# Kernel optimization log

Measured on AMD Instinct MI355X. Metric: run time of the kernel, lower is better.

## Reference

```python
import jax, jax.numpy as jnp
import numpy as np

B, N, L = 32, 1024, 128
K, D_E, H = 3, 16, 4


def setup_inputs() -> dict:
    key = jax.random.key(0)
    ks = jax.random.split(key, 7)
    return {
        "x": jax.random.normal(ks[0], (B, N, L), jnp.float32),
        # mild scaling on embeddings/projections keeps softmax logits in a sane range
        "psi_emb": jax.random.normal(ks[1], (N, D_E), jnp.float32) * 0.3,
        "psi": jnp.float32(1.0),
        "W_q": jax.random.normal(ks[2], (D_E, H, D_E), jnp.float32) * 0.2,
        "W_k": jax.random.normal(ks[3], (D_E, H, D_E), jnp.float32) * 0.2,
        "attn_alpha": jnp.float32(0.5),
        "F_w": jax.random.normal(ks[4], (H, D_E, K + 1, L), jnp.float32) * 0.1,
        "f_b": jax.random.normal(ks[5], (H, D_E), jnp.float32),
        "head_mix": jnp.ones((H,), jnp.float32),
    }


def reference(x, psi_emb, psi, W_q, W_k, attn_alpha, F_w, f_b, head_mix):
    # x: (B, N, L)
    n = x.shape[1]
    # --- gaussian adjacency: softmax over columns of exp(-psi * ||psi_i - psi_j||^2)
    diff = psi_emb[:, None, :] - psi_emb[None, :, :]          # (N, N, d_e)
    dist2 = jnp.sum(diff * diff, axis=-1)                     # (N, N)
    A_base = jax.nn.softmax(jnp.exp(-psi * dist2), axis=1)    # (N, N)
    # --- per-head attention adjacency
    Q = jnp.einsum('nd,dhm->nhm', psi_emb, W_q)               # (N, H, d_e)
    Kt = jnp.einsum('nd,dhm->nhm', psi_emb, W_k)              # (N, H, d_e)
    scale = 1.0 / jnp.sqrt(jnp.asarray(Q.shape[-1], x.dtype))
    A_attn = jax.nn.softmax(
        jnp.einsum('nhd,mhd->hnm', Q, Kt) * scale, axis=-1)   # (H, N, N)
    # --- sigmoid blend (all heads at once)
    alpha = jax.nn.sigmoid(attn_alpha)
    A_eff = alpha * A_base[None] + (1.0 - alpha) * A_attn     # (H, N, N)
    # --- Chebyshev recursion: T0 = I, T1 = A, Tk = 2 A T_{k-1} - T_{k-2}
    I = jnp.broadcast_to(jnp.eye(n, dtype=x.dtype), A_eff.shape)
    supports = [I, A_eff]
    for _ in range(2, K + 1):
        supports.append(2.0 * jnp.einsum('hnm,hml->hnl', A_eff, supports[-1]) - supports[-2])
    S = jnp.stack(supports, axis=1)                           # (H, K+1, N, N)
    # --- per-node filters
    W_filter = jnp.einsum('nd,hdkl->hnkl', psi_emb, F_w)      # (H, N, K+1, L)
    b_filter = jnp.einsum('nd,hd->hn', psi_emb, f_b)          # (H, N)
    # --- graph conv + node-specific contraction
    x_g = jnp.einsum('hknm,bml->bhknl', S, x)                 # (B, H, K+1, N, L)
    out_h = jnp.einsum('bhknl,hnkl->bhn', x_g, W_filter) + b_filter[None]
    # --- head mixing
    mix_w = jax.nn.softmax(head_mix, axis=0)                  # (H,)
    return jnp.einsum('bhn,h->bn', out_h, mix_w)              # (B, N)
```

## Files before the change

### kernel.cpp

```cpp
#include <hip/hip_runtime.h>
#include <cstdint>

#define NN 1024
#define BB 32
#define LL 128
#define DE 16
#define HH 4
#define K1 4
#define BD 512
#define NS 524288

using bf16x8 = __attribute__((ext_vector_type(8))) short;
using f32x4  = __attribute__((ext_vector_type(4))) float;

__device__ inline unsigned short f2bf(float f) {
    unsigned u = __builtin_bit_cast(unsigned, f);
    u += 0x7FFFu + ((u >> 16) & 1u);
    return (unsigned short)(u >> 16);
}
__device__ inline float bf2f(unsigned short u) {
    return __builtin_bit_cast(float, (unsigned)u << 16);
}

struct LogitsSmem {
    float ejs[64][17];
    float eis[64][17];
    float kjs[64][64];
    float qis[4][64][17];
    float part[4][5][64];
    float wq[1024];
    float wk[1024];
};
struct XtSmem { float xs[64][128]; };

__global__ __launch_bounds__(256) void phase1(
    const float* __restrict__ psi_emb, const float* __restrict__ psi_p,
    const float* __restrict__ W_q, const float* __restrict__ W_k,
    const float* __restrict__ x, const float* __restrict__ F_w,
    short* __restrict__ bnt, short* __restrict__ ant, float* __restrict__ partials,
    short* __restrict__ xt, short* __restrict__ wtt, float* __restrict__ out)
{
    __shared__ __align__(16) char smem_raw[sizeof(LogitsSmem)];
    const int bid = blockIdx.x;
    const int tid = threadIdx.x;

    if (bid < 256) {
        LogitsSmem& S = *(LogitsSmem*)smem_raw;
        const int jb = bid & 15, ib = bid >> 4;
        const int i0 = ib * 64, j0 = jb * 64;
        {
            const int row = tid >> 2, dq = (tid & 3) * 4;
            const float4 vj = *(const float4*)(psi_emb + (j0 + row) * DE + dq);
            S.ejs[row][dq] = vj.x; S.ejs[row][dq + 1] = vj.y;
            S.ejs[row][dq + 2] = vj.z; S.ejs[row][dq + 3] = vj.w;
            const float4 vi = *(const float4*)(psi_emb + (i0 + row) * DE + dq);
            S.eis[row][dq] = vi.x; S.eis[row][dq + 1] = vi.y;
            S.eis[row][dq + 2] = vi.z; S.eis[row][dq + 3] = vi.w;
            *(float4*)&S.wq[tid * 4] = *(const float4*)(W_q + tid * 4);
            *(float4*)&S.wk[tid * 4] = *(const float4*)(W_k + tid * 4);
        }
        __syncthreads();
#pragma unroll
        for (int rep = 0; rep < 16; rep++) {
            const int idx = rep * 256 + tid;
            const int row = idx >> 6, hm = idx & 63;
            float qv = 0.f, kv = 0.f;
#pragma unroll
            for (int d = 0; d < DE; d++) {
                qv += S.eis[row][d] * S.wq[d * 64 + hm];
                kv += S.ejs[row][d] * S.wk[d * 64 + hm];
            }
            S.qis[hm >> 4][row][hm & 15] = qv;
            S.kjs[row][hm] = kv;
        }
        __syncthreads();

        const int i = tid & 63, jg = tid >> 6;
        const float psi = psi_p[0];
        float er[DE];
#pragma unroll
        for (int d = 0; d < DE; d++) er[d] = S.eis[i][d];

        float sb = 0.f, sa[HH] = {0.f, 0.f, 0.f, 0.f};
#pragma unroll
        for (int g = 0; g < 2; g++) {
            unsigned short bw[8];
#pragma unroll
            for (int r = 0; r < 8; r++) {
                const int j = jg * 16 + g * 8 + r;
                float d2 = 0.f;
#pragma unroll
                for (int d = 0; d < DE; d++) { const float t = er[d] - S.ejs[j][d]; d2 += t * t; }
                const float bn = __expf(__expf(-psi * d2));
                sb += bn;
                bw[r] = f2bf(bn);
            }
            uint4 pk;
            pk.x = bw[0] | ((unsigned)bw[1] << 16);
            pk.y = bw[2] | ((unsigned)bw[3] << 16);
            pk.z = bw[4] | ((unsigned)bw[5] << 16);
            pk.w = bw[6] | ((unsigned)bw[7] << 16);
            const size_t toff = (size_t)((j0 + jg * 16 + g * 8) >> 3) * 8192 + (size_t)(i0 + i) * 8;
            *(uint4*)(bnt + toff) = pk;
        }
#pragma unroll
        for (int h = 0; h < HH; h++) {
            float qr[DE];
#pragma unroll
            for (int m = 0; m < DE; m++) qr[m] = S.qis[h][i][m];
#pragma unroll
            for (int g = 0; g < 2; g++) {
                unsigned short aw[8];
#pragma unroll
                for (int r = 0; r < 8; r++) {
                    const int j = jg * 16 + g * 8 + r;
                    float dot = 0.f;
#pragma unroll
                    for (int m = 0; m < DE; m++) dot += qr[m] * S.kjs[j][h * DE + m];
                    const float an = __expf(dot * 0.25f);
                    sa[h] += an;
                    aw[r] = f2bf(an);
                }
                uint4 pk;
                pk.x = aw[0] | ((unsigned)aw[1] << 16);
                pk.y = aw[2] | ((unsigned)aw[3] << 16);
                pk.z = aw[4] | ((unsigned)aw[5] << 16);
                pk.w = aw[6] | ((unsigned)aw[7] << 16);
                const size_t toff = (size_t)((j0 + jg * 16 + g * 8) >> 3) * 8192 + (size_t)(i0 + i) * 8;
                *(uint4*)(ant + (size_t)h * 1048576 + toff) = pk;
            }
        }
        S.part[jg][0][i] = sb;
#pragma unroll
        for (int h = 0; h < HH; h++) S.part[jg][1 + h][i] = sa[h];
        __syncthreads();
        if (tid < 64) {
#pragma unroll
            for (int s = 0; s < 5; s++) {
                const float v = S.part[0][s][tid] + S.part[1][s][tid] +
                                S.part[2][s][tid] + S.part[3][s][tid];
                partials[(size_t)jb * 5120 + (size_t)s * 1024 + i0 + tid] = v;
            }
        }
    } else if (bid < 768) {
        XtSmem& X = *(XtSmem*)smem_raw;
        const int idx = bid - 256;
        const int m0 = (idx & 15) * 64;
        const int b  = idx >> 4;
        for (int i = tid; i < 2048; i += 256) {
            const int row = i >> 5, lq = i & 31;
            *(float4*)&X.xs[row][lq * 4] =
                *(const float4*)(x + ((size_t)(b * NN + m0 + row)) * LL + lq * 4);
        }
        __syncthreads();
        for (int j = tid; j < 1024; j += 256) {
            const int m = j & 63, lc = j >> 6;
            const float* s = &X.xs[m][lc * 8];
            uint4 pk;
            pk.x = f2bf(s[0]) | ((unsigned)f2bf(s[1]) << 16);
            pk.y = f2bf(s[2]) | ((unsigned)f2bf(s[3]) << 16);
            pk.z = f2bf(s[4]) | ((unsigned)f2bf(s[5]) << 16);
            pk.w = f2bf(s[6]) | ((unsigned)f2bf(s[7]) << 16);
            *(uint4*)(xt + (size_t)b * 131072 + (size_t)lc * 8192 + (size_t)(m0 + m) * 8) = pk;
        }
    } else if (bid < 784) {
        const int j = (bid - 768) * 256 + tid;
        const int lc = j >> 8, c = j & 255;
        const int h = c >> 6, k = (c >> 4) & 3, d = c & 15;
        const float* s = F_w + (size_t)((h * DE + d) * K1 + k) * LL + lc * 8;
        uint4 pk;
        pk.x = f2bf(s[0]) | ((unsigned)f2bf(s[1]) << 16);
        pk.y = f2bf(s[2]) | ((unsigned)f2bf(s[3]) << 16);
        pk.z = f2bf(s[4]) | ((unsigned)f2bf(s[5]) << 16);
        pk.w = f2bf(s[6]) | ((unsigned)f2bf(s[7]) << 16);
        *(uint4*)(wtt + (size_t)lc * 2048 + (size_t)c * 8) = pk;
    } else {
        const int idx = (bid - 784) * 256 + tid;
        const float4 z = {0.f, 0.f, 0.f, 0.f};
        *(float4*)(out + (size_t)idx * 8) = z;
        *(float4*)(out + (size_t)idx * 8 + 4) = z;
    }
}

__global__ __launch_bounds__(256) void phase2(
    const short* __restrict__ xt, const short* __restrict__ wtt,
    short* __restrict__ Gt,
    const short* __restrict__ bnt, const short* __restrict__ ant,
    const float* __restrict__ partials, const float* __restrict__ alpha_p,
    short* __restrict__ At)
{
    const int bid = blockIdx.x;
    const int tid = threadIdx.x;
    __shared__ float sums_l[5][64];

    if (bid < 1024) {
        const int cb = bid & 3;
        const int m0 = ((bid >> 2) & 15) * 64;
        const int bp = bid >> 6;
        const int wave = tid >> 6, lane = tid & 63;
        const int b  = bp * 2 + (wave >> 1);
        const int wc = wave & 1;
        const int q = lane >> 4, m16 = lane & 15;
        const short* xb = xt + (size_t)b * 131072;

        f32x4 acc[4][2];
#pragma unroll
        for (int mi = 0; mi < 4; mi++)
#pragma unroll
            for (int ni = 0; ni < 2; ni++) acc[mi][ni] = (f32x4){0.f, 0.f, 0.f, 0.f};

#pragma unroll
        for (int ks = 0; ks < 4; ks++) {
            const int kc = ks * 4 + q;
            bf16x8 a[4], bb[2];
#pragma unroll
            for (int mi = 0; mi < 4; mi++)
                a[mi] = *(const bf16x8*)(xb + (size_t)kc * 8192 + (size_t)(m0 + mi * 16 + m16) * 8);
#pragma unroll
            for (int ni = 0; ni < 2; ni++)
                bb[ni] = *(const bf16x8*)(wtt + (size_t)kc * 2048 +
                                          (size_t)(cb * 64 + wc * 32 + ni * 16 + m16) * 8);
#pragma unroll
            for (int mi = 0; mi < 4; mi++)
#pragma unroll
                for (int ni = 0; ni < 2; ni++)
                    acc[mi][ni] = __builtin_amdgcn_mfma_f32_16x16x32_bf16(a[mi], bb[ni], acc[mi][ni], 0, 0, 0);
        }

#pragma unroll
        for (int ni = 0; ni < 2; ni++) {
            const int cc = cb * 64 + wc * 32 + ni * 16 + m16;
            const int kk = (cc >> 4) & 3, hh = cc >> 6;
            const int col512 = b * 16 + (cc & 15);
            short* gdst = Gt + (size_t)(kk * 4 + hh) * 524288;
#pragma unroll
            for (int mi = 0; mi < 4; mi++) {
                const int row0 = m0 + mi * 16 + q * 4;
                ushort4 pk;
                pk.x = f2bf(acc[mi][ni][0]); pk.y = f2bf(acc[mi][ni][1]);
                pk.z = f2bf(acc[mi][ni][2]); pk.w = f2bf(acc[mi][ni][3]);
                *(ushort4*)(gdst + ((size_t)(row0 >> 3) * 512 + col512) * 8 + (row0 & 7)) = pk;
            }
        }
    } else {
        const int idx = bid - 1024;
        const int jb = idx & 15, ib = idx >> 4;
        const int i0 = ib * 64, j0 = jb * 64;
        const int lane = tid & 63, w = tid >> 6;
        {
            float acc = 0.f;
#pragma unroll
            for (int jb2 = 0; jb2 < 16; jb2++)
                acc += partials[(size_t)jb2 * 5120 + (size_t)w * 1024 + i0 + lane];
            sums_l[w][lane] = acc;
            if (w == 0) {
                float a4 = 0.f;
#pragma unroll
                for (int jb2 = 0; jb2 < 16; jb2++)
                    a4 += partials[(size_t)jb2 * 5120 + 4 * 1024 + i0 + lane];
                sums_l[4][lane] = a4;
            }
        }
        __syncthreads();
        const int i = lane, jg = w;
        const float alpha = 1.f / (1.f + __expf(-alpha_p[0]));
        const float ibs = alpha / sums_l[0][i];
        float ias[HH];
#pragma unroll
        for (int h = 0; h < HH; h++) ias[h] = (1.f - alpha) / sums_l[1 + h][i];

#pragma unroll
        for (int g = 0; g < 2; g++) {
            const size_t toff = (size_t)((j0 + jg * 16 + g * 8) >> 3) * 8192 + (size_t)(i0 + i) * 8;
            const uint4 bp = *(const uint4*)(bnt + toff);
            float bnv[8];
            bnv[0] = bf2f(bp.x & 0xFFFF); bnv[1] = bf2f(bp.x >> 16);
            bnv[2] = bf2f(bp.y & 0xFFFF); bnv[3] = bf2f(bp.y >> 16);
            bnv[4] = bf2f(bp.z & 0xFFFF); bnv[5] = bf2f(bp.z >> 16);
            bnv[6] = bf2f(bp.w & 0xFFFF); bnv[7] = bf2f(bp.w >> 16);
#pragma unroll
            for (int h = 0; h < HH; h++) {
                const uint4 ap = *(const uint4*)(ant + (size_t)h * 1048576 + toff);
                float av[8];
                av[0] = bf2f(ap.x & 0xFFFF); av[1] = bf2f(ap.x >> 16);
                av[2] = bf2f(ap.y & 0xFFFF); av[3] = bf2f(ap.y >> 16);
                av[4] = bf2f(ap.z & 0xFFFF); av[5] = bf2f(ap.z >> 16);
                av[6] = bf2f(ap.w & 0xFFFF); av[7] = bf2f(ap.w >> 16);
                unsigned short ow[8];
#pragma unroll
                for (int r = 0; r < 8; r++) ow[r] = f2bf(ibs * bnv[r] + ias[h] * av[r]);
                uint4 pk;
                pk.x = ow[0] | ((unsigned)ow[1] << 16);
                pk.y = ow[2] | ((unsigned)ow[3] << 16);
                pk.z = ow[4] | ((unsigned)ow[5] << 16);
                pk.w = ow[6] | ((unsigned)ow[7] << 16);
                *(uint4*)(At + (size_t)h * 1048576 + toff) = pk;
            }
        }
    }
}

__global__ __launch_bounds__(256) void gemm_mf(
    const short* __restrict__ At, const short* __restrict__ Bt,
    const short* __restrict__ Pt, const short* __restrict__ Qt,
    short* __restrict__ Ot, float scale, float pc, float qc)
{
    const int bid = blockIdx.x;
    const int h = (bid & 7) >> 1;
    const int tile = ((bid >> 3) << 1) | (bid & 1);
    const int c0 = (tile & 7) * 64;
    const int r0 = (tile >> 3) * 64;

    const short* Ah = At + (size_t)h * 1048576;
    const short* Bh = Bt + (size_t)h * 524288;
    const short* Ph = Pt + (size_t)h * 524288;
    const short* Qh = Qt + (size_t)h * 524288;
    short* Oh = Ot + (size_t)h * 524288;

    const int tid = threadIdx.x;
    const int wave = tid >> 6, lane = tid & 63;
    const int q = lane >> 4, m16 = lane & 15;
    const int wr = wave >> 1, wc = wave & 1;

    const short* Ap = Ah + (size_t)q * 8192 + (size_t)(r0 + wr * 32 + m16) * 8;
    const short* Bp = Bh + (size_t)q * 4096 + (size_t)(c0 + wc * 32 + m16) * 8;

    f32x4 acc[2][2];
#pragma unroll
    for (int mi = 0; mi < 2; mi++)
#pragma unroll
        for (int ni = 0; ni < 2; ni++) acc[mi][ni] = (f32x4){0.f, 0.f, 0.f, 0.f};

#pragma unroll 8
    for (int it = 0; it < 32; it++) {
        const bf16x8 af0 = *(const bf16x8*)(Ap + (size_t)it * 32768);
        const bf16x8 af1 = *(const bf16x8*)(Ap + (size_t)it * 32768 + 128);
        const bf16x8 bf0 = *(const bf16x8*)(Bp + (size_t)it * 16384);
        const bf16x8 bf1 = *(const bf16x8*)(Bp + (size_t)it * 16384 + 128);
        acc[0][0] = __builtin_amdgcn_mfma_f32_16x16x32_bf16(af0, bf0, acc[0][0], 0, 0, 0);
        acc[0][1] = __builtin_amdgcn_mfma_f32_16x16x32_bf16(af0, bf1, acc[0][1], 0, 0, 0);
        acc[1][0] = __builtin_amdgcn_mfma_f32_16x16x32_bf16(af1, bf0, acc[1][0], 0, 0, 0);
        acc[1][1] = __builtin_amdgcn_mfma_f32_16x16x32_bf16(af1, bf1, acc[1][1], 0, 0, 0);
    }

#pragma unroll
    for (int mi = 0; mi < 2; mi++) {
        const int row0 = r0 + wr * 32 + mi * 16 + q * 4;
#pragma unroll
        for (int ni = 0; ni < 2; ni++) {
            const int cc = c0 + wc * 32 + ni * 16 + m16;
            const size_t off = ((size_t)(row0 >> 3) * 512 + cc) * 8 + (row0 & 7);
            const ushort4 pv = *(const ushort4*)(Ph + off);
            float v[4];
            v[0] = scale * acc[mi][ni][0] + pc * bf2f(pv.x);
            v[1] = scale * acc[mi][ni][1] + pc * bf2f(pv.y);
            v[2] = scale * acc[mi][ni][2] + pc * bf2f(pv.z);
            v[3] = scale * acc[mi][ni][3] + pc * bf2f(pv.w);
            if (qc != 0.f) {
                const ushort4 qv = *(const ushort4*)(Qh + off);
                v[0] += qc * bf2f(qv.x); v[1] += qc * bf2f(qv.y);
                v[2] += qc * bf2f(qv.z); v[3] += qc * bf2f(qv.w);
            }
            ushort4 pk;
            pk.x = f2bf(v[0]); pk.y = f2bf(v[1]); pk.z = f2bf(v[2]); pk.w = f2bf(v[3]);
            *(ushort4*)(Oh + off) = pk;
        }
    }
}

__global__ __launch_bounds__(256) void gemm3_out(
    const short* __restrict__ At, const short* __restrict__ Bt,
    const short* __restrict__ Pt, const short* __restrict__ Qt,
    const float* __restrict__ psi_emb, const float* __restrict__ f_b,
    const float* __restrict__ head_mix, float* __restrict__ out)
{
    const int bid = blockIdx.x;
    const int h = (bid & 7) >> 1;
    const int tile = ((bid >> 3) << 1) | (bid & 1);
    const int c0 = (tile & 7) * 64;
    const int r0 = (tile >> 3) * 64;

    const short* Ah = At + (size_t)h * 1048576;
    const short* Bh = Bt + (size_t)h * 524288;
    const short* Ph = Pt + (size_t)h * 524288;
    const short* Qh = Qt + (size_t)h * 524288;

    const int tid = threadIdx.x;
    const int wave = tid >> 6, lane = tid & 63;
    const int q = lane >> 4, m16 = lane & 15;
    const int wr = wave >> 1, wc = wave & 1;

    __shared__ float es[64][17];
    {
        const int row = tid >> 2, dq = (tid & 3) * 4;
        const float4 ev = *(const float4*)(psi_emb + (size_t)(r0 + row) * DE + dq);
        es[row][dq] = ev.x; es[row][dq + 1] = ev.y;
        es[row][dq + 2] = ev.z; es[row][dq + 3] = ev.w;
    }
    __syncthreads();

    const short* Ap = Ah + (size_t)q * 8192 + (size_t)(r0 + wr * 32 + m16) * 8;
    const short* Bp = Bh + (size_t)q * 4096 + (size_t)(c0 + wc * 32 + m16) * 8;

    f32x4 acc[2][2];
#pragma unroll
    for (int mi = 0; mi < 2; mi++)
#pragma unroll
        for (int ni = 0; ni < 2; ni++) acc[mi][ni] = (f32x4){0.f, 0.f, 0.f, 0.f};

#pragma unroll 8
    for (int it = 0; it < 32; it++) {
        const bf16x8 af0 = *(const bf16x8*)(Ap + (size_t)it * 32768);
        const bf16x8 af1 = *(const bf16x8*)(Ap + (size_t)it * 32768 + 128);
        const bf16x8 bf0 = *(const bf16x8*)(Bp + (size_t)it * 16384);
        const bf16x8 bf1 = *(const bf16x8*)(Bp + (size_t)it * 16384 + 128);
        acc[0][0] = __builtin_amdgcn_mfma_f32_16x16x32_bf16(af0, bf0, acc[0][0], 0, 0, 0);
        acc[0][1] = __builtin_amdgcn_mfma_f32_16x16x32_bf16(af0, bf1, acc[0][1], 0, 0, 0);
        acc[1][0] = __builtin_amdgcn_mfma_f32_16x16x32_bf16(af1, bf0, acc[1][0], 0, 0, 0);
        acc[1][1] = __builtin_amdgcn_mfma_f32_16x16x32_bf16(af1, bf1, acc[1][1], 0, 0, 0);
    }

    const float hm0 = head_mix[0], hm1 = head_mix[1], hm2 = head_mix[2], hm3 = head_mix[3];
    const float mx = fmaxf(fmaxf(hm0, hm1), fmaxf(hm2, hm3));
    const float w0 = expf(hm0 - mx), w1 = expf(hm1 - mx), w2 = expf(hm2 - mx), w3 = expf(hm3 - mx);
    const float isum = 1.f / (w0 + w1 + w2 + w3);
    const float mwh = (h == 0 ? w0 : h == 1 ? w1 : h == 2 ? w2 : w3) * isum;
    const float fb = f_b[h * DE + m16];

#pragma unroll
    for (int mi = 0; mi < 2; mi++) {
        const int rloc0 = wr * 32 + mi * 16 + q * 4;
        const int row0 = r0 + rloc0;
#pragma unroll
        for (int ni = 0; ni < 2; ni++) {
            const int cc = c0 + wc * 32 + ni * 16 + m16;
            const int b = cc >> 4;
            const size_t off = ((size_t)(row0 >> 3) * 512 + cc) * 8 + (row0 & 7);
            const ushort4 pv = *(const ushort4*)(Ph + off);
            const ushort4 qv = *(const ushort4*)(Qh + off);
            float v[4];
            v[0] = acc[mi][ni][0] + bf2f(pv.x) - bf2f(qv.x);
            v[1] = acc[mi][ni][1] + bf2f(pv.y) - bf2f(qv.y);
            v[2] = acc[mi][ni][2] + bf2f(pv.z) - bf2f(qv.z);
            v[3] = acc[mi][ni][3] + bf2f(pv.w) - bf2f(qv.w);
#pragma unroll
            for (int r = 0; r < 4; r++) {
                float w = es[rloc0 + r][m16] * (v[r] + fb);
                w += __shfl_xor(w, 1, 64);
                w += __shfl_xor(w, 2, 64);
                w += __shfl_xor(w, 4, 64);
                w += __shfl_xor(w, 8, 64);
                if (m16 == 0)
                    atomicAdd(out + (size_t)b * NN + (row0 + r), mwh * w);
            }
        }
    }
}

extern "C" void kernel_launch(void* const* d_in, const int* in_sizes, int n_in,
                              void* d_out, int out_size, void* d_ws, size_t ws_size,
                              hipStream_t stream)
{
    const float* x          = (const float*)d_in[0];
    const float* psi_emb    = (const float*)d_in[1];
    const float* psi        = (const float*)d_in[2];
    const float* W_q        = (const float*)d_in[3];
    const float* W_k        = (const float*)d_in[4];
    const float* attn_alpha = (const float*)d_in[5];
    const float* F_w        = (const float*)d_in[6];
    const float* f_b        = (const float*)d_in[7];
    const float* head_mix   = (const float*)d_in[8];
    float* out = (float*)d_out;

    short* At  = (short*)d_ws;
    short* xt  = At + 4194304;
    short* wtt = xt + 4194304;
    short* Gt  = wtt + 32768;
    short* b2t = Gt + 8388608;
    short* b1t = b2t + 2097152;
    short* bnt = b1t + 2097152;
    short* ant = bnt + 1048576;
    float* partials = (float*)(ant + 4194304);

    const size_t need_bytes =
        (size_t)(4194304 + 4194304 + 32768 + 8388608 + 2097152 + 2097152 + 1048576 + 4194304) * 2 +
        (size_t)81920 * 4;
    if (ws_size < need_bytes) return;

    phase1<<<800, 256, 0, stream>>>(psi_emb, psi, W_q, W_k, x, F_w,
                                    bnt, ant, partials, xt, wtt, out);
    phase2<<<1280, 256, 0, stream>>>(xt, wtt, Gt, bnt, ant, partials,
                                     attn_alpha, At);

    gemm_mf<<<512, 256, 0, stream>>>(At, Gt + 12 * (size_t)524288, Gt + 8 * (size_t)524288,
                                     Gt , b2t, 2.f, 1.f, 0.f);
    gemm_mf<<<512, 256, 0, stream>>>(At, b2t, Gt + 4 * (size_t)524288,
                                     Gt + 12 * (size_t)524288, b1t, 2.f, 1.f, -1.f);
    gemm3_out<<<512, 256, 0, stream>>>(At, b1t, Gt, b2t, psi_emb, f_b, head_mix, out);
}
```

Measured before the change: 148.6 us.

## Fuse three Clenshaw GEMM launches into one cooperative kernel with grid syncs

Replaces the two gemm_mf launches and the final gemm3_out launch with one cooperative kernel. It runs the three A·B products back to back and separates them with grid-wide barriers. The goal is to remove kernel launch gaps and tail effects between the dependent steps. The cost is grid.sync overhead, and the cooperative launch needs all 512 blocks resident at once, or it fails.

```diff
diff --git a/kernel.cpp b/kernel.cpp
--- a/kernel.cpp
+++ b/kernel.cpp
@@ -1,5 +1,8 @@
 #include <hip/hip_runtime.h>
+#include <hip/hip_cooperative_groups.h>
 #include <cstdint>
+
+namespace cg = cooperative_groups;
 
 #define NN 1024
 #define BB 32
@@ -8,7 +11,7 @@
 #define HH 4
 #define K1 4
 #define BD 512
-#define NS 524288
+#define SLAB 524288
 
 using bf16x8 = __attribute__((ext_vector_type(8))) short;
 using f32x4  = __attribute__((ext_vector_type(4))) float;
@@ -232,7 +235,7 @@
             const int cc = cb * 64 + wc * 32 + ni * 16 + m16;
             const int kk = (cc >> 4) & 3, hh = cc >> 6;
             const int col512 = b * 16 + (cc & 15);
-            short* gdst = Gt + (size_t)(kk * 4 + hh) * 524288;
+            short* gdst = Gt + (size_t)(kk * 4 + hh) * SLAB;
 #pragma unroll
             for (int mi = 0; mi < 4; mi++) {
                 const int row0 = m0 + mi * 16 + q * 4;
@@ -300,37 +303,11 @@
     }
 }
 
-__global__ __launch_bounds__(256) void gemm_mf(
-    const short* __restrict__ At, const short* __restrict__ Bt,
-    const short* __restrict__ Pt, const short* __restrict__ Qt,
-    short* __restrict__ Ot, float scale, float pc, float qc)
-{
-    const int bid = blockIdx.x;
-    const int h = (bid & 7) >> 1;
-    const int tile = ((bid >> 3) << 1) | (bid & 1);
-    const int c0 = (tile & 7) * 64;
-    const int r0 = (tile >> 3) * 64;
-
-    const short* Ah = At + (size_t)h * 1048576;
-    const short* Bh = Bt + (size_t)h * 524288;
-    const short* Ph = Pt + (size_t)h * 524288;
-    const short* Qh = Qt + (size_t)h * 524288;
-    short* Oh = Ot + (size_t)h * 524288;
-
-    const int tid = threadIdx.x;
-    const int wave = tid >> 6, lane = tid & 63;
-    const int q = lane >> 4, m16 = lane & 15;
-    const int wr = wave >> 1, wc = wave & 1;
-
-    const short* Ap = Ah + (size_t)q * 8192 + (size_t)(r0 + wr * 32 + m16) * 8;
-    const short* Bp = Bh + (size_t)q * 4096 + (size_t)(c0 + wc * 32 + m16) * 8;
-
-    f32x4 acc[2][2];
+__device__ inline void k_loop(const short* Ap, const short* Bp, f32x4 acc[2][2]) {
 #pragma unroll
     for (int mi = 0; mi < 2; mi++)
 #pragma unroll
         for (int ni = 0; ni < 2; ni++) acc[mi][ni] = (f32x4){0.f, 0.f, 0.f, 0.f};
-
 #pragma unroll 8
     for (int it = 0; it < 32; it++) {
         const bf16x8 af0 = *(const bf16x8*)(Ap + (size_t)it * 32768);
@@ -342,53 +319,31 @@
         acc[1][0] = __builtin_amdgcn_mfma_f32_16x16x32_bf16(af1, bf0, acc[1][0], 0, 0, 0);
         acc[1][1] = __builtin_amdgcn_mfma_f32_16x16x32_bf16(af1, bf1, acc[1][1], 0, 0, 0);
     }
-
-#pragma unroll
-    for (int mi = 0; mi < 2; mi++) {
-        const int row0 = r0 + wr * 32 + mi * 16 + q * 4;
-#pragma unroll
-        for (int ni = 0; ni < 2; ni++) {
-            const int cc = c0 + wc * 32 + ni * 16 + m16;
-            const size_t off = ((size_t)(row0 >> 3) * 512 + cc) * 8 + (row0 & 7);
-            const ushort4 pv = *(const ushort4*)(Ph + off);
-            float v[4];
-            v[0] = scale * acc[mi][ni][0] + pc * bf2f(pv.x);
-            v[1] = scale * acc[mi][ni][1] + pc * bf2f(pv.y);
-            v[2] = scale * acc[mi][ni][2] + pc * bf2f(pv.z);
-            v[3] = scale * acc[mi][ni][3] + pc * bf2f(pv.w);
-            if (qc != 0.f) {
-                const ushort4 qv = *(const ushort4*)(Qh + off);
-                v[0] += qc * bf2f(qv.x); v[1] += qc * bf2f(qv.y);
-                v[2] += qc * bf2f(qv.z); v[3] += qc * bf2f(qv.w);
-            }
-            ushort4 pk;
-            pk.x = f2bf(v[0]); pk.y = f2bf(v[1]); pk.z = f2bf(v[2]); pk.w = f2bf(v[3]);
-            *(ushort4*)(Oh + off) = pk;
-        }
-    }
-}
-
-__global__ __launch_bounds__(256) void gemm3_out(
-    const short* __restrict__ At, const short* __restrict__ Bt,
-    const short* __restrict__ Pt, const short* __restrict__ Qt,
+}
+
+__global__ __launch_bounds__(256) void clenshaw_chain(
+    const short* __restrict__ At, const short* __restrict__ Gt,
+    short* b2t, short* b1t,
     const float* __restrict__ psi_emb, const float* __restrict__ f_b,
     const float* __restrict__ head_mix, float* __restrict__ out)
 {
+    cg::grid_group grid = cg::this_grid();
+
     const int bid = blockIdx.x;
     const int h = (bid & 7) >> 1;
     const int tile = ((bid >> 3) << 1) | (bid & 1);
     const int c0 = (tile & 7) * 64;
     const int r0 = (tile >> 3) * 64;
 
-    const short* Ah = At + (size_t)h * 1048576;
-    const short* Bh = Bt + (size_t)h * 524288;
-    const short* Ph = Pt + (size_t)h * 524288;
-    const short* Qh = Qt + (size_t)h * 524288;
-
     const int tid = threadIdx.x;
     const int wave = tid >> 6, lane = tid & 63;
     const int q = lane >> 4, m16 = lane & 15;
     const int wr = wave >> 1, wc = wave & 1;
+
+    const size_t hs = (size_t)h * SLAB;
+    const short* Ap = At + (size_t)h * 1048576 +
+                      (size_t)q * 8192 + (size_t)(r0 + wr * 32 + m16) * 8;
+    const size_t bofs = (size_t)q * 4096 + (size_t)(c0 + wc * 32 + m16) * 8;
 
     __shared__ float es[64][17];
     {
@@ -399,26 +354,50 @@
     }
     __syncthreads();
 
-    const short* Ap = Ah + (size_t)q * 8192 + (size_t)(r0 + wr * 32 + m16) * 8;
-    const short* Bp = Bh + (size_t)q * 4096 + (size_t)(c0 + wc * 32 + m16) * 8;
-
     f32x4 acc[2][2];
-#pragma unroll
-    for (int mi = 0; mi < 2; mi++)
-#pragma unroll
-        for (int ni = 0; ni < 2; ni++) acc[mi][ni] = (f32x4){0.f, 0.f, 0.f, 0.f};
-
-#pragma unroll 8
-    for (int it = 0; it < 32; it++) {
-        const bf16x8 af0 = *(const bf16x8*)(Ap + (size_t)it * 32768);
-        const bf16x8 af1 = *(const bf16x8*)(Ap + (size_t)it * 32768 + 128);
-        const bf16x8 bf0 = *(const bf16x8*)(Bp + (size_t)it * 16384);
-        const bf16x8 bf1 = *(const bf16x8*)(Bp + (size_t)it * 16384 + 128);
-        acc[0][0] = __builtin_amdgcn_mfma_f32_16x16x32_bf16(af0, bf0, acc[0][0], 0, 0, 0);
-        acc[0][1] = __builtin_amdgcn_mfma_f32_16x16x32_bf16(af0, bf1, acc[0][1], 0, 0, 0);
-        acc[1][0] = __builtin_amdgcn_mfma_f32_16x16x32_bf16(af1, bf0, acc[1][0], 0, 0, 0);
-        acc[1][1] = __builtin_amdgcn_mfma_f32_16x16x32_bf16(af1, bf1, acc[1][1], 0, 0, 0);
-    }
+
+    k_loop(Ap, Gt + (12 + h) * (size_t)SLAB + bofs, acc);
+#pragma unroll
+    for (int mi = 0; mi < 2; mi++) {
+        const int row0 = r0 + wr * 32 + mi * 16 + q * 4;
+#pragma unroll
+        for (int ni = 0; ni < 2; ni++) {
+            const int cc = c0 + wc * 32 + ni * 16 + m16;
+            const size_t off = ((size_t)(row0 >> 3) * 512 + cc) * 8 + (row0 & 7);
+            const ushort4 pv = *(const ushort4*)(Gt + (8 + h) * (size_t)SLAB + off);
+            ushort4 pk;
+            pk.x = f2bf(2.f * acc[mi][ni][0] + bf2f(pv.x));
+            pk.y = f2bf(2.f * acc[mi][ni][1] + bf2f(pv.y));
+            pk.z = f2bf(2.f * acc[mi][ni][2] + bf2f(pv.z));
+            pk.w = f2bf(2.f * acc[mi][ni][3] + bf2f(pv.w));
+            *(ushort4*)(b2t + hs + off) = pk;
+        }
+    }
+    __threadfence();
+    grid.sync();
+
+    k_loop(Ap, b2t + hs + bofs, acc);
+#pragma unroll
+    for (int mi = 0; mi < 2; mi++) {
+        const int row0 = r0 + wr * 32 + mi * 16 + q * 4;
+#pragma unroll
+        for (int ni = 0; ni < 2; ni++) {
+            const int cc = c0 + wc * 32 + ni * 16 + m16;
+            const size_t off = ((size_t)(row0 >> 3) * 512 + cc) * 8 + (row0 & 7);
+            const ushort4 pv = *(const ushort4*)(Gt + (4 + h) * (size_t)SLAB + off);
+            const ushort4 qv = *(const ushort4*)(Gt + (12 + h) * (size_t)SLAB + off);
+            ushort4 pk;
+            pk.x = f2bf(2.f * acc[mi][ni][0] + bf2f(pv.x) - bf2f(qv.x));
+            pk.y = f2bf(2.f * acc[mi][ni][1] + bf2f(pv.y) - bf2f(qv.y));
+            pk.z = f2bf(2.f * acc[mi][ni][2] + bf2f(pv.z) - bf2f(qv.z));
+            pk.w = f2bf(2.f * acc[mi][ni][3] + bf2f(pv.w) - bf2f(qv.w));
+            *(ushort4*)(b1t + hs + off) = pk;
+        }
+    }
+    __threadfence();
+    grid.sync();
+
+    k_loop(Ap, b1t + hs + bofs, acc);
 
     const float hm0 = head_mix[0], hm1 = head_mix[1], hm2 = head_mix[2], hm3 = head_mix[3];
     const float mx = fmaxf(fmaxf(hm0, hm1), fmaxf(hm2, hm3));
@@ -436,8 +415,8 @@
             const int cc = c0 + wc * 32 + ni * 16 + m16;
             const int b = cc >> 4;
             const size_t off = ((size_t)(row0 >> 3) * 512 + cc) * 8 + (row0 & 7);
-            const ushort4 pv = *(const ushort4*)(Ph + off);
-            const ushort4 qv = *(const ushort4*)(Qh + off);
+            const ushort4 pv = *(const ushort4*)(Gt + (0 + h) * (size_t)SLAB + off);
+            const ushort4 qv = *(const ushort4*)(b2t + hs + off);
             float v[4];
             v[0] = acc[mi][ni][0] + bf2f(pv.x) - bf2f(qv.x);
             v[1] = acc[mi][ni][1] + bf2f(pv.y) - bf2f(qv.y);
@@ -492,9 +471,8 @@
     phase2<<<1280, 256, 0, stream>>>(xt, wtt, Gt, bnt, ant, partials,
                                      attn_alpha, At);
 
-    gemm_mf<<<512, 256, 0, stream>>>(At, Gt + 12 * (size_t)524288, Gt + 8 * (size_t)524288,
-                                     Gt , b2t, 2.f, 1.f, 0.f);
-    gemm_mf<<<512, 256, 0, stream>>>(At, b2t, Gt + 4 * (size_t)524288,
-                                     Gt + 12 * (size_t)524288, b1t, 2.f, 1.f, -1.f);
-    gemm3_out<<<512, 256, 0, stream>>>(At, b1t, Gt, b2t, psi_emb, f_b, head_mix, out);
-}
+    void* args[] = {(void*)&At, (void*)&Gt, (void*)&b2t, (void*)&b1t,
+                    (void*)&psi_emb, (void*)&f_b, (void*)&head_mix, (void*)&out};
+    hipLaunchCooperativeKernel((const void*)clenshaw_chain, dim3(512), dim3(256),
+                               args, 0, stream);
+}
```

New measurement: 380.6 us. 2.56x slower.
